# Performance work log

Hardware: AMD Instinct MI355X
Metric: run time of the kernel (lower is better)

## Reference

```python
import jax, jax.numpy as jnp
import numpy as np

S, N, D, F, E = 2048, 8, 1024, 4096, 8
STD = 0.02


def setup_inputs() -> dict:
    key = jax.random.key(0)
    ks = jax.random.split(key, 5)
    x = jax.random.normal(ks[0], (S, N, D), dtype=jnp.float32)
    Wg = jax.random.normal(ks[1], (E, D), dtype=jnp.float32) * STD
    W1 = jax.random.normal(ks[2], (E, F, D), dtype=jnp.float32) * STD
    b1 = jnp.zeros((E, F), dtype=jnp.float32)
    W2 = jax.random.normal(ks[3], (E, D, F), dtype=jnp.float32) * STD
    b2 = jnp.zeros((E, D), dtype=jnp.float32)
    return {"x": x, "Wg": Wg, "W1": W1, "b1": b1, "W2": W2, "b2": b2}


def reference(x, Wg, W1, b1, W2, b2):
    # Gate (eval mode: no gating noise). scores: [S, N, E]
    scores = jnp.einsum('snd,ed->sne', x, Wg)
    prob = jax.nn.softmax(scores, axis=-1)
    top1_idx = jnp.argmax(prob, axis=-1)                                   # [S, N] int
    top1_prob = jnp.take_along_axis(prob, top1_idx[..., None], axis=-1)[..., 0]  # [S, N]

    y = jnp.zeros_like(x)
    n_experts = Wg.shape[0]
    for e in range(n_experts):  # small fixed loop over experts
        h = jax.nn.gelu(jnp.einsum('snd,fd->snf', x, W1[e]) + b1[e], approximate=False)
        ye = jnp.einsum('snf,df->snd', h, W2[e]) + b2[e]
        mask = (top1_idx == e)[..., None]                                  # [S, N, 1]
        y = y + jnp.where(mask, ye * top1_prob[..., None], 0.0)
    return y
```

## Files before the change

### kernel.cpp

```cpp
#include <hip/hip_runtime.h>

#define S_TOK 16384
#define D_DIM 1024
#define F_DIM 4096
#define E_NUM 8

#define BM 128
#define BN 128
#define BK 64
#define MT_MAX 136

typedef short bf16x8 __attribute__((ext_vector_type(8)));
typedef float f32x4 __attribute__((ext_vector_type(4)));
typedef unsigned short ushort_t;

static __device__ __forceinline__ unsigned short f32_bf16(float f) {
  unsigned u = __float_as_uint(f);
  return (unsigned short)((u + 0x7FFFu + ((u >> 16) & 1u)) >> 16);
}

static __device__ __forceinline__ unsigned int pack_bf16x2(float a, float b) {
  unsigned ua = __float_as_uint(a);
  unsigned ub = __float_as_uint(b);
  unsigned lo = (ua + 0x7FFFu + ((ua >> 16) & 1u)) >> 16;
  unsigned hi = (ub + 0x7FFFu + ((ub >> 16) & 1u)) & 0xFFFF0000u;
  return lo | hi;
}

static __device__ __forceinline__ uint2 cvt_f4_bf4(const float4 v) {
  uint2 r;
  r.x = pack_bf16x2(v.x, v.y);
  r.y = pack_bf16x2(v.z, v.w);
  return r;
}

static __device__ __forceinline__ void load_lds16(const void* g, void* l) {
  __builtin_amdgcn_global_load_lds(g, l, 16, 0, 0);
}

__global__ void zero_counts_kernel(int* counts) {
  if (threadIdx.x < E_NUM) counts[threadIdx.x] = 0;
}

__global__ void cast2_kernel(const float* __restrict__ w1, ushort_t* __restrict__ o1,
                             const float* __restrict__ w2, ushort_t* __restrict__ o2) {
  const int half = 16384;
  const float* src = (blockIdx.x < half) ? w1 : w2;
  ushort_t* dst = (blockIdx.x < half) ? o1 : o2;
  const int b = (blockIdx.x < half) ? blockIdx.x : (blockIdx.x - half);
  const size_t base = ((size_t)b * blockDim.x + threadIdx.x) * 8;
  const float4 v0 = *(const float4*)(src + base);
  const float4 v1 = *(const float4*)(src + base + 4);
  const uint2 a = cvt_f4_bf4(v0), c = cvt_f4_bf4(v1);
  uint4 w; w.x = a.x; w.y = a.y; w.z = c.x; w.w = c.y;
  *(uint4*)(dst + base) = w;
}

__global__ void gate_kernel(const float* __restrict__ x,
                            const float* __restrict__ Wg,
                            ushort_t* __restrict__ xbf,
                            float* __restrict__ prob,
                            int* __restrict__ counts,
                            int* __restrict__ tok_list) {
  const int wv = threadIdx.x >> 6;
  const int lane = threadIdx.x & 63;
  const int t = blockIdx.x * 4 + wv;
  const float* xr = x + (size_t)t * D_DIM;
  ushort_t* xb = xbf + (size_t)t * D_DIM;

  float acc[E_NUM];
#pragma unroll
  for (int e = 0; e < E_NUM; ++e) acc[e] = 0.0f;

#pragma unroll
  for (int i = 0; i < 4; ++i) {
    const int k = i * 256 + lane * 4;
    const float4 v = *(const float4*)(xr + k);
    *(uint2*)(xb + k) = cvt_f4_bf4(v);
#pragma unroll
    for (int e = 0; e < E_NUM; ++e) {
      const float4 w = *(const float4*)(Wg + e * D_DIM + k);
      acc[e] += v.x * w.x + v.y * w.y + v.z * w.z + v.w * w.w;
    }
  }
#pragma unroll
  for (int e = 0; e < E_NUM; ++e) {
#pragma unroll
    for (int off = 32; off > 0; off >>= 1)
      acc[e] += __shfl_xor(acc[e], off, 64);
  }
  if (lane == 0) {
    float m = acc[0]; int bi = 0;
#pragma unroll
    for (int e = 1; e < E_NUM; ++e) {
      if (acc[e] > m) { m = acc[e]; bi = e; }
    }
    float s = 0.0f;
#pragma unroll
    for (int e = 0; e < E_NUM; ++e) s += expf(acc[e] - m);
    prob[t] = 1.0f / s;
    int p = atomicAdd(&counts[bi], 1);
    tok_list[bi * S_TOK + p] = t;
  }
}

__global__ void plan_kernel(const int* __restrict__ counts, int* __restrict__ plan) {
  if (threadIdx.x == 0) {
    int t = 0;
    for (int e = 0; e < E_NUM; ++e) {
      const int nt = (counts[e] + BM - 1) / BM;
      for (int i = 0; i < nt; ++i) {
        plan[1 + t] = e;
        plan[1 + MT_MAX + t] = i * BM;
        ++t;
      }
    }
    plan[0] = t;
  }
}

template <int KDIM, int NDIM, int EPI>
__launch_bounds__(256, 4)
__global__ void ffn_kernel(const ushort_t* __restrict__ A,
                           const ushort_t* __restrict__ B,
                           const float* __restrict__ bias,
                           const float* __restrict__ prob,
                           const int* __restrict__ counts,
                           const int* __restrict__ tok_list,
                           const int* __restrict__ plan,
                           ushort_t* __restrict__ Hout,
                           float* __restrict__ out) {
  constexpr int NT = NDIM / BN;
  constexpr int NK = KDIM / BK;
  const int ntiles = plan[0];
  const int live = ntiles * NT;
  if (blockIdx.x >= live) return;
  const int q = live >> 3, r = live & 7;
  const int xcd = blockIdx.x & 7, idx = blockIdx.x >> 3;
  const int wg = (xcd < r ? xcd * (q + 1) : r * (q + 1) + (xcd - r) * q) + idx;
  const int tile = wg / NT;
  const int n0 = (wg % NT) * BN;
  const int e = plan[1 + tile];
  const int m0 = plan[1 + MT_MAX + tile];
  const int cnt = counts[e];

  __shared__ ushort_t As[BM * BK];
  __shared__ ushort_t Bs[BM * BK];

  const int tid = threadIdx.x;
  const int lane = tid & 63;
  const int w = tid >> 6;
  const int wr = (w >> 1) * 64;
  const int wc = (w & 1) * 64;
  const int l15 = lane & 15;
  const int l4  = lane >> 4;

  const int sub = lane >> 3;
  const int sslot = ((lane & 7) ^ sub) * 8;
  const int dstoff = w * 2048;

  const size_t ebase = (size_t)e * S_TOK;
  const ushort_t* Be = B + (size_t)e * NDIM * KDIM;
  const ushort_t* pA[4];
  const ushort_t* pB[4];
#pragma unroll
  for (int j = 0; j < 4; ++j) {
    const int ra = m0 + w * 32 + j * 8 + sub;
    const int tok = (ra < cnt) ? tok_list[ebase + ra] : 0;
    pA[j] = A + (size_t)tok * KDIM + sslot;
    pB[j] = Be + (size_t)(n0 + w * 32 + j * 8 + sub) * KDIM + sslot;
  }

  int oA[4][2], oB[4][2];
#pragma unroll
  for (int m = 0; m < 4; ++m) {
    const int rr = wr + m * 16 + l15;
#pragma unroll
    for (int kk = 0; kk < 2; ++kk)
      oA[m][kk] = rr * BK + (((kk * 4 + l4) ^ (rr & 7)) * 8);
  }
#pragma unroll
  for (int n = 0; n < 4; ++n) {
    const int rr = wc + n * 16 + l15;
#pragma unroll
    for (int kk = 0; kk < 2; ++kk)
      oB[n][kk] = rr * BK + (((kk * 4 + l4) ^ (rr & 7)) * 8);
  }

  f32x4 acc[4][4];
#pragma unroll
  for (int i = 0; i < 4; ++i)
#pragma unroll
    for (int j = 0; j < 4; ++j)
      acc[i][j] = (f32x4){0.f, 0.f, 0.f, 0.f};

  for (int t = 0; t < NK; ++t) {
    const int k0 = t * BK;
#pragma unroll
    for (int j = 0; j < 4; ++j) {
      load_lds16(pA[j] + k0, &As[dstoff + j * 512]);
      load_lds16(pB[j] + k0, &Bs[dstoff + j * 512]);
    }
    __syncthreads();

#pragma unroll
    for (int kk = 0; kk < 2; ++kk) {
      bf16x8 a[4], b[4];
#pragma unroll
      for (int i = 0; i < 4; ++i) {
        a[i] = *(const bf16x8*)&As[oA[i][kk]];
        b[i] = *(const bf16x8*)&Bs[oB[i][kk]];
      }
#pragma unroll
      for (int mi = 0; mi < 4; ++mi)
#pragma unroll
        for (int ni = 0; ni < 4; ++ni)
          acc[mi][ni] = __builtin_amdgcn_mfma_f32_16x16x32_bf16(a[mi], b[ni], acc[mi][ni], 0, 0, 0);
    }

    __syncthreads();
  }

  const float* be = bias + (size_t)e * NDIM;
#pragma unroll
  for (int mi = 0; mi < 4; ++mi) {
#pragma unroll
    for (int rr = 0; rr < 4; ++rr) {
      const int slot = m0 + wr + mi * 16 + l4 * 4 + rr;
      if (slot >= cnt) continue;
      const int tok = tok_list[ebase + slot];
      if (EPI == 0) {
        ushort_t* hrow = Hout + (size_t)tok * NDIM;
#pragma unroll
        for (int ni = 0; ni < 4; ++ni) {
          const int col = n0 + wc + ni * 16 + l15;
          float v = acc[mi][ni][rr] + be[col];
          v = 0.5f * v * (1.0f + erff(v * 0.70710678118654752f));
          hrow[col] = f32_bf16(v);
        }
      } else {
        const float p = prob[tok];
        float* orow = out + (size_t)tok * NDIM;
#pragma unroll
        for (int ni = 0; ni < 4; ++ni) {
          const int col = n0 + wc + ni * 16 + l15;
          orow[col] = (acc[mi][ni][rr] + be[col]) * p;
        }
      }
    }
  }
}

extern "C" void kernel_launch(void* const* d_in, const int* in_sizes, int n_in,
                              void* d_out, int out_size, void* d_ws, size_t ws_size,
                              hipStream_t stream) {
  const float* x  = (const float*)d_in[0];
  const float* Wg = (const float*)d_in[1];
  const float* W1 = (const float*)d_in[2];
  const float* b1 = (const float*)d_in[3];
  const float* W2 = (const float*)d_in[4];
  const float* b2 = (const float*)d_in[5];
  float* out = (float*)d_out;

  const size_t MB = 1ull << 20;
  char* ws = (char*)d_ws;
  int* counts      = (int*)(ws);
  int* plan        = (int*)(ws + 4096);
  float* prob      = (float*)(ws + 64 * 1024);
  int* tok_list    = (int*)(ws + 128 * 1024);
  ushort_t* xbf    = (ushort_t*)(ws + 1 * MB);
  ushort_t* W1bf   = (ushort_t*)(ws + 33 * MB);
  ushort_t* W2bf   = (ushort_t*)(ws + 97 * MB);
  ushort_t* H      = (ushort_t*)(ws + 161 * MB);

  zero_counts_kernel<<<1, 64, 0, stream>>>(counts);
  gate_kernel<<<S_TOK / 4, 256, 0, stream>>>(x, Wg, xbf, prob, counts, tok_list);
  plan_kernel<<<1, 64, 0, stream>>>(counts, plan);

  cast2_kernel<<<32768, 256, 0, stream>>>(W1, W1bf, W2, W2bf);

  ffn_kernel<D_DIM, F_DIM, 0><<<(F_DIM / BN) * MT_MAX, 256, 0, stream>>>(
      xbf, W1bf, b1, nullptr, counts, tok_list, plan, H, nullptr);

  ffn_kernel<F_DIM, D_DIM, 1><<<(D_DIM / BN) * MT_MAX, 256, 0, stream>>>(
      H, W2bf, b2, prob, counts, tok_list, plan, nullptr, out);
}
```

Before: 709.3 us.

## Double-buffer LDS tiles in expert FFN GEMM and use polynomial erf for GELU

The expert GEMM kernel now keeps two LDS buffers and issues the global-to-LDS loads for tile t+1 before computing on tile t, so it needs one barrier per iteration instead of two and overlaps memory latency with MFMA work. Launch bounds drop from 4 to 2 waves per SIMD because LDS use doubles. The exact erff in the GELU epilogue is replaced by the Abramowitz-Stegun polynomial with __expf, which is cheaper but only accurate to about 1e-7 absolute. There is a risk of a race: the prefetch into the next buffer is issued before the current buffer is read, and only one barrier separates iterations.

```diff
diff --git a/kernel.cpp b/kernel.cpp
--- a/kernel.cpp
+++ b/kernel.cpp
@@ -36,6 +36,16 @@
 
 static __device__ __forceinline__ void load_lds16(const void* g, void* l) {
   __builtin_amdgcn_global_load_lds(g, l, 16, 0, 0);
+}
+
+static __device__ __forceinline__ float gelu_f(float v) {
+  const float u = fabsf(v) * 0.70710678118654752f;
+  const float t = 1.0f / (1.0f + 0.3275911f * u);
+  const float poly = t * (0.254829592f + t * (-0.284496736f + t * (1.421413741f +
+                     t * (-1.453152027f + t * 1.061405429f))));
+  const float erfa = 1.0f - poly * __expf(-u * u);
+  const float erfv = (v >= 0.0f) ? erfa : -erfa;
+  return 0.5f * v * (1.0f + erfv);
 }
 
 __global__ void zero_counts_kernel(int* counts) {
@@ -120,7 +130,7 @@
 }
 
 template <int KDIM, int NDIM, int EPI>
-__launch_bounds__(256, 4)
+__launch_bounds__(256, 2)
 __global__ void ffn_kernel(const ushort_t* __restrict__ A,
                            const ushort_t* __restrict__ B,
                            const float* __restrict__ bias,
@@ -144,8 +154,8 @@
   const int m0 = plan[1 + MT_MAX + tile];
   const int cnt = counts[e];
 
-  __shared__ ushort_t As[BM * BK];
-  __shared__ ushort_t Bs[BM * BK];
+  __shared__ ushort_t As[2][BM * BK];
+  __shared__ ushort_t Bs[2][BM * BK];
 
   const int tid = threadIdx.x;
   const int lane = tid & 63;
@@ -194,22 +204,32 @@
     for (int j = 0; j < 4; ++j)
       acc[i][j] = (f32x4){0.f, 0.f, 0.f, 0.f};
 
+#pragma unroll
+  for (int j = 0; j < 4; ++j) {
+    load_lds16(pA[j], &As[0][dstoff + j * 512]);
+    load_lds16(pB[j], &Bs[0][dstoff + j * 512]);
+  }
+  __syncthreads();
+
+  int cb = 0;
   for (int t = 0; t < NK; ++t) {
-    const int k0 = t * BK;
-#pragma unroll
-    for (int j = 0; j < 4; ++j) {
-      load_lds16(pA[j] + k0, &As[dstoff + j * 512]);
-      load_lds16(pB[j] + k0, &Bs[dstoff + j * 512]);
-    }
-    __syncthreads();
+    if (t + 1 < NK) {
+      const int k0 = (t + 1) * BK;
+      const int nb = cb ^ 1;
+#pragma unroll
+      for (int j = 0; j < 4; ++j) {
+        load_lds16(pA[j] + k0, &As[nb][dstoff + j * 512]);
+        load_lds16(pB[j] + k0, &Bs[nb][dstoff + j * 512]);
+      }
+    }
 
 #pragma unroll
     for (int kk = 0; kk < 2; ++kk) {
       bf16x8 a[4], b[4];
 #pragma unroll
       for (int i = 0; i < 4; ++i) {
-        a[i] = *(const bf16x8*)&As[oA[i][kk]];
-        b[i] = *(const bf16x8*)&Bs[oB[i][kk]];
+        a[i] = *(const bf16x8*)&As[cb][oA[i][kk]];
+        b[i] = *(const bf16x8*)&Bs[cb][oB[i][kk]];
       }
 #pragma unroll
       for (int mi = 0; mi < 4; ++mi)
@@ -219,6 +239,7 @@
     }
 
     __syncthreads();
+    cb ^= 1;
   }
 
   const float* be = bias + (size_t)e * NDIM;
@@ -234,9 +255,7 @@
 #pragma unroll
         for (int ni = 0; ni < 4; ++ni) {
           const int col = n0 + wc + ni * 16 + l15;
-          float v = acc[mi][ni][rr] + be[col];
-          v = 0.5f * v * (1.0f + erff(v * 0.70710678118654752f));
-          hrow[col] = f32_bf16(v);
+          hrow[col] = f32_bf16(gelu_f(acc[mi][ni][rr] + be[col]));
         }
       } else {
         const float p = prob[tok];
```

Result: slower. 831.4 us (+17.2%).
